# Optimization experiments

Measured on AMD Instinct MI355X. Metric: run time of the kernel, lower is better.

Reference implementation:

```python
import jax, jax.numpy as jnp
import numpy as np

N_NODES = 100000
N_EDGES = 600000
DIM = 128  # 2 * size_in


def gcn_layer(x, W, b, src, dst, n):
    # GCNConv (PyG, normalize=True, add_self_loops=True):
    # h = x @ W; norm = deg^-1/2[src] * deg^-1/2[dst] with self-loops; out = scatter_add + b
    h = x @ W
    loops = jnp.arange(n)
    s = jnp.concatenate([src, loops])
    d = jnp.concatenate([dst, loops])
    deg = jax.ops.segment_sum(jnp.ones_like(s, dtype=x.dtype), d, num_segments=n)
    dinv = jnp.where(deg > 0, deg ** -0.5, 0.0).astype(x.dtype)
    norm = dinv[s] * dinv[d]  # [E+N]
    msg = h[s] * norm[:, None]  # [E+N, DIM] -- dominant gather traffic
    out = jax.ops.segment_sum(msg, d, num_segments=n)
    return out + b


def setup_inputs() -> dict:
    key = jax.random.key(0)
    k = jax.random.split(key, 6)
    x = jax.random.normal(k[0], (N_NODES, DIM), dtype=jnp.float32)
    W1 = jax.random.normal(k[1], (DIM, DIM), dtype=jnp.float32) * (DIM ** -0.5)
    b1 = jax.random.normal(k[2], (DIM,), dtype=jnp.float32) * 0.02
    W2 = jax.random.normal(k[3], (DIM, DIM), dtype=jnp.float32) * (DIM ** -0.5)
    b2 = jax.random.normal(k[4], (DIM,), dtype=jnp.float32) * 0.02
    edge_index = jax.random.randint(k[5], (2, N_EDGES), 0, N_NODES, dtype=jnp.int64 if jax.config.jax_enable_x64 else jnp.int32)
    return {"x": x, "W1": W1, "b1": b1, "W2": W2, "b2": b2, "edge_index": edge_index}


def reference(x, W1, b1, W2, b2, edge_index):
    src, dst = edge_index[0], edge_index[1]
    out = gcn_layer(x, W1, b1, src, dst, N_NODES)
    out = jnp.tanh(out)
    out = gcn_layer(out, W2, b2, src, dst, N_NODES)
    return out
```

## Files before the change

### kernel.cpp

```cpp
#include <hip/hip_runtime.h>
#include <math.h>

#define NBLK 256

typedef __attribute__((ext_vector_type(8))) short short8v;
typedef __attribute__((ext_vector_type(4))) float f32x4;

__device__ __forceinline__ unsigned cvt_pk_bf16(float lo, float hi) {
    unsigned r;
    asm("v_cvt_pk_bf16_f32 %0, %1, %2" : "=v"(r) : "v"(lo), "v"(hi));
    return r;
}
__device__ __forceinline__ float bf_lo(unsigned u) { return __uint_as_float(u << 16); }
__device__ __forceinline__ float bf_hi(unsigned u) { return __uint_as_float(u & 0xffff0000u); }

__device__ __forceinline__ float fast_tanh(float x) {
    float cx = fminf(fmaxf(x, -15.f), 15.f);
    float e = __expf(2.f * cx);
    return (e - 1.f) / (e + 1.f);
}


__global__ __launch_bounds__(NBLK) void scan1_k(const int* __restrict__ cnt, int n,
                                                int* __restrict__ off, int* __restrict__ bsum) {
    __shared__ int ls[NBLK];
    int base = blockIdx.x * 1024 + threadIdx.x * 4;
    int v[4]; int s = 0;
#pragma unroll
    for (int i = 0; i < 4; ++i) {
        int idx = base + i;
        v[i] = (idx < n) ? cnt[idx] : 0;
        s += v[i];
    }
    ls[threadIdx.x] = s;
    __syncthreads();
    for (int o = 1; o < NBLK; o <<= 1) {
        int t = (threadIdx.x >= (unsigned)o) ? ls[threadIdx.x - o] : 0;
        __syncthreads();
        ls[threadIdx.x] += t;
        __syncthreads();
    }
    int run = ls[threadIdx.x] - s;
#pragma unroll
    for (int i = 0; i < 4; ++i) {
        int idx = base + i;
        if (idx < n) off[idx] = run;
        run += v[i];
    }
    if (threadIdx.x == NBLK - 1) bsum[blockIdx.x] = ls[NBLK - 1];
}

__global__ void scan2_k(int* bsum, int nb) {
    __shared__ int ls[128];
    int t = threadIdx.x;
    int v = (t < nb) ? bsum[t] : 0;
    ls[t] = v;
    __syncthreads();
    for (int o = 1; o < 128; o <<= 1) {
        int tv = (t >= o) ? ls[t - o] : 0;
        __syncthreads();
        ls[t] += tv;
        __syncthreads();
    }
    if (t < nb) bsum[t] = ls[t] - v;
}

__global__ __launch_bounds__(NBLK) void scan3_k(int* __restrict__ off, const int* __restrict__ bsum,
                                                const int* __restrict__ cnt,
                                                float* __restrict__ dinv, int n) {
    int i = blockIdx.x * blockDim.x + threadIdx.x;
    if (i < n) {
        off[i] += bsum[i >> 10];
        dinv[i] = rsqrtf((float)(cnt[i] + 1));
    }
}

__global__ __launch_bounds__(NBLK) void fill2_k(const int* __restrict__ src, const int* __restrict__ dst, int E,
                                                const int* __restrict__ off, const int* __restrict__ pos,
                                                int* __restrict__ srcs) {
    int e = blockIdx.x * blockDim.x + threadIdx.x;
    if (e >= E) return;
    srcs[off[dst[e]] + pos[e]] = src[e];
}

__global__ __launch_bounds__(NBLK) void wcast_k(const float* __restrict__ W1, const float* __restrict__ W2,
                                                ushort* __restrict__ Wt1, ushort* __restrict__ Wt2) {
    int i = blockIdx.x * blockDim.x + threadIdx.x;
    int which = i >> 14;
    int idx = i & 16383;
    const float* W = which ? W2 : W1;
    ushort* Wt = which ? Wt2 : Wt1;
    int k = idx >> 7, c = idx & 127;
    float v = W[idx];
    Wt[c * 128 + k] = (ushort)(cvt_pk_bf16(v, v) & 0xffffu);
}


template<int CVT, int DINV, int DO_COUNT>
__global__ __launch_bounds__(NBLK, 4) void gemm_mfma_k(const void* __restrict__ Xin,
                                                       const ushort* __restrict__ Wt,
                                                       const float* __restrict__ dinv,
                                                       ushort* __restrict__ Gb, int nrows,
                                                       const int* __restrict__ dste,
                                                       int* __restrict__ cntp,
                                                       int* __restrict__ posp, int E) {
    __shared__ unsigned Xls[64 * 64];
    __shared__ unsigned Wls[128 * 64];
    const int t = threadIdx.x;
    const int lane = t & 63;
    const int wv = t >> 6;
    const int l15 = lane & 15;
    const int g = lane >> 4;
    const int row0 = blockIdx.x * 64;

    {
        const uint4* Wv = (const uint4*)Wt;
        for (int i = t; i < 2048; i += NBLK) {
            int col = i >> 4, ku = i & 15;
            *(uint4*)&Wls[(col * 16 + (ku ^ (col & 15))) * 4] = Wv[i];
        }
    }
    {
        int r = t >> 2;
        int rg = row0 + r;
#pragma unroll
        for (int j = 0; j < 4; ++j) {
            int u = (t & 3) + 4 * j;
            uint4 val;
            if (CVT) {
                float4 f0 = make_float4(0.f,0.f,0.f,0.f), f1 = f0;
                if (rg < nrows) {
                    const float4* Xv = (const float4*)Xin;
                    f0 = Xv[(size_t)rg * 32 + u * 2];
                    f1 = Xv[(size_t)rg * 32 + u * 2 + 1];
                }
                val.x = cvt_pk_bf16(f0.x, f0.y); val.y = cvt_pk_bf16(f0.z, f0.w);
                val.z = cvt_pk_bf16(f1.x, f1.y); val.w = cvt_pk_bf16(f1.z, f1.w);
            } else {
                val = make_uint4(0u,0u,0u,0u);
                if (rg < nrows) val = ((const uint4*)Xin)[(size_t)rg * 16 + u];
            }
            *(uint4*)&Xls[(r * 16 + (u ^ (r & 15))) * 4] = val;
        }
    }
    __syncthreads();

    short8v A[4];
#pragma unroll
    for (int ks = 0; ks < 4; ++ks) {
        int r = wv * 16 + l15;
        int u = ks * 4 + g;
        A[ks] = *(short8v*)&Xls[(r * 16 + (u ^ (r & 15))) * 4];
    }

    f32x4 acc[8];
#pragma unroll
    for (int nt = 0; nt < 8; ++nt) acc[nt] = (f32x4){0.f, 0.f, 0.f, 0.f};
#pragma unroll
    for (int nt = 0; nt < 8; ++nt) {
        int col = nt * 16 + l15;
#pragma unroll
        for (int ks = 0; ks < 4; ++ks) {
            int ku = ks * 4 + g;
            short8v b = *(short8v*)&Wls[(col * 16 + (ku ^ (col & 15))) * 4];
            acc[nt] = __builtin_amdgcn_mfma_f32_16x16x32_bf16(A[ks], b, acc[nt], 0, 0, 0);
        }
    }

    int trow0 = row0 + wv * 16;
    float dv[4];
#pragma unroll
    for (int q = 0; q < 4; ++q) {
        int row = trow0 + g * 4 + q;
        dv[q] = DINV ? ((row < nrows) ? dinv[row] : 0.f) : 1.f;
    }
#pragma unroll
    for (int nt = 0; nt < 8; ++nt)
#pragma unroll
        for (int q = 0; q < 4; ++q) {
            int row = trow0 + g * 4 + q;
            if (row < nrows) {
                float val = DINV ? acc[nt][q] * dv[q] : acc[nt][q];
                Gb[(size_t)row * 128 + nt * 16 + l15] =
                    (ushort)(cvt_pk_bf16(val, val) & 0xffffu);
            }
        }

    if (DO_COUNT) {
        int stride = gridDim.x * NBLK;
        for (int e = blockIdx.x * NBLK + t; e < E; e += stride)
            posp[e] = atomicAdd(&cntp[dste[e]], 1);
    }
}


#define UPK_FMA(u4, nm, A) { \
    A[0] = fmaf(bf_lo((u4).x), (nm), A[0]); A[1] = fmaf(bf_hi((u4).x), (nm), A[1]); \
    A[2] = fmaf(bf_lo((u4).y), (nm), A[2]); A[3] = fmaf(bf_hi((u4).y), (nm), A[3]); \
    A[4] = fmaf(bf_lo((u4).z), (nm), A[4]); A[5] = fmaf(bf_hi((u4).z), (nm), A[5]); \
    A[6] = fmaf(bf_lo((u4).w), (nm), A[6]); A[7] = fmaf(bf_hi((u4).w), (nm), A[7]); }

template<int SRC_DINV, int TANH_, int OUT_BF16>
__global__ __launch_bounds__(NBLK, 4) void aggregate_k(const ushort* __restrict__ Gb,
                                                       const int* __restrict__ off, const int* __restrict__ cnt,
                                                       const int* __restrict__ srcs,
                                                       const float* __restrict__ dinv,
                                                       const float* __restrict__ bias,
                                                       void* __restrict__ outp, int n) {
    int node = (blockIdx.x * blockDim.x + threadIdx.x) >> 4;
    if (node >= n) return;
    int il = threadIdx.x & 15;

    const uint4* Gv = (const uint4*)Gb;
    float dvn = dinv[node];
    float sw = SRC_DINV ? dvn : 1.f;
    uint4 s0 = Gv[(size_t)node * 16 + il];
    float acc[8] = {
        bf_lo(s0.x) * sw, bf_hi(s0.x) * sw, bf_lo(s0.y) * sw, bf_hi(s0.y) * sw,
        bf_lo(s0.z) * sw, bf_hi(s0.z) * sw, bf_lo(s0.w) * sw, bf_hi(s0.w) * sw
    };

    int e0 = off[node];
    int deg = cnt[node];
    for (int b = 0; b < deg; b += 8) {
        int sidx[8]; float nm[8];
#pragma unroll
        for (int q = 0; q < 8; ++q) {
            bool v = (b + q) < deg;
            sidx[q] = v ? srcs[e0 + b + q] : node;
            nm[q] = v ? 1.f : 0.f;
        }
        if (SRC_DINV) {
#pragma unroll
            for (int q = 0; q < 8; ++q) nm[q] *= dinv[sidx[q]];
        }
        uint4 gr[8];
#pragma unroll
        for (int q = 0; q < 8; ++q) gr[q] = Gv[(size_t)sidx[q] * 16 + il];
#pragma unroll
        for (int q = 0; q < 8; ++q) UPK_FMA(gr[q], nm[q], acc);
    }

    float4 b0 = *(const float4*)&bias[il * 8];
    float4 b1 = *(const float4*)&bias[il * 8 + 4];
    float r[8];
    r[0] = fmaf(acc[0], dvn, b0.x); r[1] = fmaf(acc[1], dvn, b0.y);
    r[2] = fmaf(acc[2], dvn, b0.z); r[3] = fmaf(acc[3], dvn, b0.w);
    r[4] = fmaf(acc[4], dvn, b1.x); r[5] = fmaf(acc[5], dvn, b1.y);
    r[6] = fmaf(acc[6], dvn, b1.z); r[7] = fmaf(acc[7], dvn, b1.w);

    if (TANH_) {
#pragma unroll
        for (int i = 0; i < 8; ++i) r[i] = fast_tanh(r[i]);
    }

    if (OUT_BF16) {
        uint4 o;
        o.x = cvt_pk_bf16(r[0], r[1]); o.y = cvt_pk_bf16(r[2], r[3]);
        o.z = cvt_pk_bf16(r[4], r[5]); o.w = cvt_pk_bf16(r[6], r[7]);
        ((uint4*)outp)[(size_t)node * 16 + il] = o;
    } else {
        float* O = (float*)outp;
        *(float4*)&O[(size_t)node * 128 + il * 8]     = make_float4(r[0], r[1], r[2], r[3]);
        *(float4*)&O[(size_t)node * 128 + il * 8 + 4] = make_float4(r[4], r[5], r[6], r[7]);
    }
}


extern "C" void kernel_launch(void* const* d_in, const int* in_sizes, int n_in,
                              void* d_out, int out_size, void* d_ws, size_t ws_size,
                              hipStream_t stream) {
    const float* x  = (const float*)d_in[0];
    const float* W1 = (const float*)d_in[1];
    const float* b1 = (const float*)d_in[2];
    const float* W2 = (const float*)d_in[3];
    const float* b2 = (const float*)d_in[4];
    const int*   ei = (const int*)d_in[5];

    const int N = in_sizes[0] / 128;
    const int E = in_sizes[5] / 2;
    const int* src = ei;
    const int* dst = ei + E;

    char* p = (char*)d_ws;
    ushort* gb    = (ushort*)p; p += (size_t)N * 128 * sizeof(ushort);
    ushort* tb    = (ushort*)p; p += (size_t)N * 128 * sizeof(ushort);
    int*    cnt   = (int*)p;    p += (size_t)N * sizeof(int);
    int*    off   = (int*)p;    p += (size_t)N * sizeof(int);
    float*  dinv  = (float*)p;  p += (size_t)N * sizeof(float);
    int*    srcs  = (int*)p;    p += (size_t)E * sizeof(int);
    int*    pos   = (int*)p;    p += (size_t)E * sizeof(int);
    ushort* Wt1   = (ushort*)p; p += 16384 * sizeof(ushort);
    ushort* Wt2   = (ushort*)p; p += 16384 * sizeof(ushort);
    int*    bsum  = (int*)p;    p += 1024;

    const int nb  = (N + 1023) / 1024;
    const int nbt = (N + 63) / 64;
    const int agg_blocks = ((size_t)N * 16 + NBLK - 1) / NBLK;

    hipMemsetAsync(cnt, 0, (size_t)N * sizeof(int), stream);
    wcast_k<<<128, NBLK, 0, stream>>>(W1, W2, Wt1, Wt2);

    gemm_mfma_k<1, 0, 1><<<nbt, NBLK, 0, stream>>>(x, Wt1, nullptr, gb, N, dst, cnt, pos, E);

    scan1_k<<<nb, NBLK, 0, stream>>>(cnt, N, off, bsum);
    scan2_k<<<1, 128, 0, stream>>>(bsum, nb);
    scan3_k<<<(N + NBLK - 1) / NBLK, NBLK, 0, stream>>>(off, bsum, cnt, dinv, N);
    fill2_k<<<(E + NBLK - 1) / NBLK, NBLK, 0, stream>>>(src, dst, E, off, pos, srcs);

    aggregate_k<1, 1, 1><<<agg_blocks, NBLK, 0, stream>>>(gb, off, cnt, srcs, dinv, b1, tb, N);
    gemm_mfma_k<0, 1, 0><<<nbt, NBLK, 0, stream>>>(tb, Wt2, dinv, gb, N, nullptr, nullptr, nullptr, 0);
    aggregate_k<0, 0, 0><<<agg_blocks, NBLK, 0, stream>>>(gb, off, cnt, srcs, dinv, b2, d_out, N);
}
```

Before: 168.4 us.

## Split degree-count atomics across eight per-block-group counter slices

The edge-degree counting atomics in the first GEMM now go to one of eight counter arrays chosen by block index, with the slice id packed into the per-edge position. The scan sums the eight slices, and a new pass turns each slice into a base offset and writes a separate degree array, which the fill and aggregate kernels use. The aim is to cut atomic contention on the same counter addresses. In exchange it adds an 8x larger memset and extra strided reads and writes in the scan kernels.

```diff
diff --git a/kernel.cpp b/kernel.cpp
--- a/kernel.cpp
+++ b/kernel.cpp
@@ -21,7 +21,7 @@
 }
 
 
-__global__ __launch_bounds__(NBLK) void scan1_k(const int* __restrict__ cnt, int n,
+__global__ __launch_bounds__(NBLK) void scan1_k(const int* __restrict__ cnt8, int n,
                                                 int* __restrict__ off, int* __restrict__ bsum) {
     __shared__ int ls[NBLK];
     int base = blockIdx.x * 1024 + threadIdx.x * 4;
@@ -29,8 +29,13 @@
 #pragma unroll
     for (int i = 0; i < 4; ++i) {
         int idx = base + i;
-        v[i] = (idx < n) ? cnt[idx] : 0;
-        s += v[i];
+        int d = 0;
+        if (idx < n) {
+#pragma unroll
+            for (int x = 0; x < 8; ++x) d += cnt8[(size_t)x * n + idx];
+        }
+        v[i] = d;
+        s += d;
     }
     ls[threadIdx.x] = s;
     __syncthreads();
@@ -66,21 +71,33 @@
 }
 
 __global__ __launch_bounds__(NBLK) void scan3_k(int* __restrict__ off, const int* __restrict__ bsum,
-                                                const int* __restrict__ cnt,
+                                                int* __restrict__ cnt8, int* __restrict__ deg,
                                                 float* __restrict__ dinv, int n) {
     int i = blockIdx.x * blockDim.x + threadIdx.x;
     if (i < n) {
-        off[i] += bsum[i >> 10];
-        dinv[i] = rsqrtf((float)(cnt[i] + 1));
+        int o = off[i] + bsum[i >> 10];
+        off[i] = o;
+        int run = o;
+#pragma unroll
+        for (int x = 0; x < 8; ++x) {
+            size_t idx = (size_t)x * n + i;
+            int c = cnt8[idx];
+            cnt8[idx] = run;
+            run += c;
+        }
+        int d = run - o;
+        deg[i] = d;
+        dinv[i] = rsqrtf((float)(d + 1));
     }
 }
 
 __global__ __launch_bounds__(NBLK) void fill2_k(const int* __restrict__ src, const int* __restrict__ dst, int E,
-                                                const int* __restrict__ off, const int* __restrict__ pos,
-                                                int* __restrict__ srcs) {
+                                                const int* __restrict__ base8, const int* __restrict__ pos,
+                                                int* __restrict__ srcs, int n) {
     int e = blockIdx.x * blockDim.x + threadIdx.x;
     if (e >= E) return;
-    srcs[off[dst[e]] + pos[e]] = src[e];
+    int pe = pos[e];
+    srcs[base8[(size_t)(pe & 7) * n + dst[e]] + (pe >> 3)] = src[e];
 }
 
 __global__ __launch_bounds__(NBLK) void wcast_k(const float* __restrict__ W1, const float* __restrict__ W2,
@@ -102,7 +119,7 @@
                                                        const float* __restrict__ dinv,
                                                        ushort* __restrict__ Gb, int nrows,
                                                        const int* __restrict__ dste,
-                                                       int* __restrict__ cntp,
+                                                       int* __restrict__ cnt8,
                                                        int* __restrict__ posp, int E) {
     __shared__ unsigned Xls[64 * 64];
     __shared__ unsigned Wls[128 * 64];
@@ -187,9 +204,11 @@
         }
 
     if (DO_COUNT) {
+        const int part = blockIdx.x & 7;
+        int* cslice = cnt8 + (size_t)part * nrows;
         int stride = gridDim.x * NBLK;
         for (int e = blockIdx.x * NBLK + t; e < E; e += stride)
-            posp[e] = atomicAdd(&cntp[dste[e]], 1);
+            posp[e] = (atomicAdd(&cslice[dste[e]], 1) << 3) | part;
     }
 }
 
@@ -202,7 +221,7 @@
 
 template<int SRC_DINV, int TANH_, int OUT_BF16>
 __global__ __launch_bounds__(NBLK, 4) void aggregate_k(const ushort* __restrict__ Gb,
-                                                       const int* __restrict__ off, const int* __restrict__ cnt,
+                                                       const int* __restrict__ off, const int* __restrict__ deg_,
                                                        const int* __restrict__ srcs,
                                                        const float* __restrict__ dinv,
                                                        const float* __restrict__ bias,
@@ -221,7 +240,7 @@
     };
 
     int e0 = off[node];
-    int deg = cnt[node];
+    int deg = deg_[node];
     for (int b = 0; b < deg; b += 8) {
         int sidx[8]; float nm[8];
 #pragma unroll
@@ -285,8 +304,9 @@
     char* p = (char*)d_ws;
     ushort* gb    = (ushort*)p; p += (size_t)N * 128 * sizeof(ushort);
     ushort* tb    = (ushort*)p; p += (size_t)N * 128 * sizeof(ushort);
-    int*    cnt   = (int*)p;    p += (size_t)N * sizeof(int);
+    int*    cnt8  = (int*)p;    p += (size_t)8 * N * sizeof(int);
     int*    off   = (int*)p;    p += (size_t)N * sizeof(int);
+    int*    deg   = (int*)p;    p += (size_t)N * sizeof(int);
     float*  dinv  = (float*)p;  p += (size_t)N * sizeof(float);
     int*    srcs  = (int*)p;    p += (size_t)E * sizeof(int);
     int*    pos   = (int*)p;    p += (size_t)E * sizeof(int);
@@ -298,17 +318,17 @@
     const int nbt = (N + 63) / 64;
     const int agg_blocks = ((size_t)N * 16 + NBLK - 1) / NBLK;
 
-    hipMemsetAsync(cnt, 0, (size_t)N * sizeof(int), stream);
+    hipMemsetAsync(cnt8, 0, (size_t)8 * N * sizeof(int), stream);
     wcast_k<<<128, NBLK, 0, stream>>>(W1, W2, Wt1, Wt2);
 
-    gemm_mfma_k<1, 0, 1><<<nbt, NBLK, 0, stream>>>(x, Wt1, nullptr, gb, N, dst, cnt, pos, E);
-
-    scan1_k<<<nb, NBLK, 0, stream>>>(cnt, N, off, bsum);
+    gemm_mfma_k<1, 0, 1><<<nbt, NBLK, 0, stream>>>(x, Wt1, nullptr, gb, N, dst, cnt8, pos, E);
+
+    scan1_k<<<nb, NBLK, 0, stream>>>(cnt8, N, off, bsum);
     scan2_k<<<1, 128, 0, stream>>>(bsum, nb);
-    scan3_k<<<(N + NBLK - 1) / NBLK, NBLK, 0, stream>>>(off, bsum, cnt, dinv, N);
-    fill2_k<<<(E + NBLK - 1) / NBLK, NBLK, 0, stream>>>(src, dst, E, off, pos, srcs);
-
-    aggregate_k<1, 1, 1><<<agg_blocks, NBLK, 0, stream>>>(gb, off, cnt, srcs, dinv, b1, tb, N);
+    scan3_k<<<(N + NBLK - 1) / NBLK, NBLK, 0, stream>>>(off, bsum, cnt8, deg, dinv, N);
+    fill2_k<<<(E + NBLK - 1) / NBLK, NBLK, 0, stream>>>(src, dst, E, cnt8, pos, srcs, N);
+
+    aggregate_k<1, 1, 1><<<agg_blocks, NBLK, 0, stream>>>(gb, off, deg, srcs, dinv, b1, tb, N);
     gemm_mfma_k<0, 1, 0><<<nbt, NBLK, 0, stream>>>(tb, Wt2, dinv, gb, N, nullptr, nullptr, nullptr, 0);
-    aggregate_k<0, 0, 0><<<agg_blocks, NBLK, 0, stream>>>(gb, off, cnt, srcs, dinv, b2, d_out, N);
-}
+    aggregate_k<0, 0, 0><<<agg_blocks, NBLK, 0, stream>>>(gb, off, deg, srcs, dinv, b2, d_out, N);
+}
```

Measured after the change: 166.0 us. Within noise of the previous version (-1.5%).

## Build CSR via range-partitioned LDS histograms and load GEMM A operand directly

Applied to the files above, without the earlier changes.

Replaces global-atomic degree counting (fused into the first GEMM) and the pos/fill pass with two kernels. In each, a block owns a contiguous range of destination nodes and scans all edges, using shared-memory atomics for counting and for placing sources. This removes the memset and the per-edge pos array, at the cost of every block rereading the full edge list with only 32 blocks active. The GEMM also loads its A fragments straight from global memory instead of staging X through LDS.

```diff
diff --git a/kernel.cpp b/kernel.cpp
--- a/kernel.cpp
+++ b/kernel.cpp
@@ -2,6 +2,9 @@
 #include <math.h>
 
 #define NBLK 256
+#define HB   32
+#define HT   1024
+#define RMAX 3200
 
 typedef __attribute__((ext_vector_type(8))) short short8v;
 typedef __attribute__((ext_vector_type(4))) float f32x4;
@@ -18,6 +21,61 @@
     float cx = fminf(fmaxf(x, -15.f), 15.f);
     float e = __expf(2.f * cx);
     return (e - 1.f) / (e + 1.f);
+}
+
+
+__global__ __launch_bounds__(HT) void count_hist_k(const int* __restrict__ dst, int E,
+                                                   int* __restrict__ cnt, int n, int R) {
+    __shared__ int hist[RMAX];
+    const int base = blockIdx.x * R;
+    for (int j = threadIdx.x; j < R; j += HT) hist[j] = 0;
+    __syncthreads();
+    const int e4 = E >> 2;
+    const int4* d4 = (const int4*)dst;
+    for (int i = threadIdx.x; i < e4; i += HT) {
+        int4 d = d4[i];
+        int v;
+        v = d.x - base; if ((unsigned)v < (unsigned)R) atomicAdd(&hist[v], 1);
+        v = d.y - base; if ((unsigned)v < (unsigned)R) atomicAdd(&hist[v], 1);
+        v = d.z - base; if ((unsigned)v < (unsigned)R) atomicAdd(&hist[v], 1);
+        v = d.w - base; if ((unsigned)v < (unsigned)R) atomicAdd(&hist[v], 1);
+    }
+    for (int e = (e4 << 2) + threadIdx.x; e < E; e += HT) {
+        int v = dst[e] - base; if ((unsigned)v < (unsigned)R) atomicAdd(&hist[v], 1);
+    }
+    __syncthreads();
+    for (int j = threadIdx.x; j < R; j += HT) {
+        int b = base + j;
+        if (b < n) cnt[b] = hist[j];
+    }
+}
+
+__global__ __launch_bounds__(HT) void fill_hist_k(const int* __restrict__ src, const int* __restrict__ dst,
+                                                  int E, const int* __restrict__ off,
+                                                  int* __restrict__ srcs, int n, int R) {
+    __shared__ int cur[RMAX];
+    const int base = blockIdx.x * R;
+    for (int j = threadIdx.x; j < R; j += HT) {
+        int b = base + j;
+        cur[j] = (b < n) ? off[b] : 0;
+    }
+    __syncthreads();
+    const int e4 = E >> 2;
+    const int4* d4 = (const int4*)dst;
+    const int4* s4 = (const int4*)src;
+    for (int i = threadIdx.x; i < e4; i += HT) {
+        int4 d = d4[i];
+        int4 s = s4[i];
+        int v;
+        v = d.x - base; if ((unsigned)v < (unsigned)R) srcs[atomicAdd(&cur[v], 1)] = s.x;
+        v = d.y - base; if ((unsigned)v < (unsigned)R) srcs[atomicAdd(&cur[v], 1)] = s.y;
+        v = d.z - base; if ((unsigned)v < (unsigned)R) srcs[atomicAdd(&cur[v], 1)] = s.z;
+        v = d.w - base; if ((unsigned)v < (unsigned)R) srcs[atomicAdd(&cur[v], 1)] = s.w;
+    }
+    for (int e = (e4 << 2) + threadIdx.x; e < E; e += HT) {
+        int v = dst[e] - base;
+        if ((unsigned)v < (unsigned)R) srcs[atomicAdd(&cur[v], 1)] = src[e];
+    }
 }
 
 
@@ -73,14 +131,6 @@
         off[i] += bsum[i >> 10];
         dinv[i] = rsqrtf((float)(cnt[i] + 1));
     }
-}
-
-__global__ __launch_bounds__(NBLK) void fill2_k(const int* __restrict__ src, const int* __restrict__ dst, int E,
-                                                const int* __restrict__ off, const int* __restrict__ pos,
-                                                int* __restrict__ srcs) {
-    int e = blockIdx.x * blockDim.x + threadIdx.x;
-    if (e >= E) return;
-    srcs[off[dst[e]] + pos[e]] = src[e];
 }
 
 __global__ __launch_bounds__(NBLK) void wcast_k(const float* __restrict__ W1, const float* __restrict__ W2,
@@ -96,15 +146,11 @@
 }
 
 
-template<int CVT, int DINV, int DO_COUNT>
+template<int CVT, int DINV>
 __global__ __launch_bounds__(NBLK, 4) void gemm_mfma_k(const void* __restrict__ Xin,
                                                        const ushort* __restrict__ Wt,
                                                        const float* __restrict__ dinv,
-                                                       ushort* __restrict__ Gb, int nrows,
-                                                       const int* __restrict__ dste,
-                                                       int* __restrict__ cntp,
-                                                       int* __restrict__ posp, int E) {
-    __shared__ unsigned Xls[64 * 64];
+                                                       ushort* __restrict__ Gb, int nrows) {
     __shared__ unsigned Wls[128 * 64];
     const int t = threadIdx.x;
     const int lane = t & 63;
@@ -120,38 +166,32 @@
             *(uint4*)&Wls[(col * 16 + (ku ^ (col & 15))) * 4] = Wv[i];
         }
     }
-    {
-        int r = t >> 2;
-        int rg = row0 + r;
-#pragma unroll
-        for (int j = 0; j < 4; ++j) {
-            int u = (t & 3) + 4 * j;
-            uint4 val;
-            if (CVT) {
-                float4 f0 = make_float4(0.f,0.f,0.f,0.f), f1 = f0;
-                if (rg < nrows) {
-                    const float4* Xv = (const float4*)Xin;
-                    f0 = Xv[(size_t)rg * 32 + u * 2];
-                    f1 = Xv[(size_t)rg * 32 + u * 2 + 1];
-                }
-                val.x = cvt_pk_bf16(f0.x, f0.y); val.y = cvt_pk_bf16(f0.z, f0.w);
-                val.z = cvt_pk_bf16(f1.x, f1.y); val.w = cvt_pk_bf16(f1.z, f1.w);
-            } else {
-                val = make_uint4(0u,0u,0u,0u);
-                if (rg < nrows) val = ((const uint4*)Xin)[(size_t)rg * 16 + u];
-            }
-            *(uint4*)&Xls[(r * 16 + (u ^ (r & 15))) * 4] = val;
-        }
-    }
-    __syncthreads();
-
+
+    int arow = row0 + wv * 16 + l15;
+    int ar = (arow < nrows) ? arow : 0;
     short8v A[4];
-#pragma unroll
-    for (int ks = 0; ks < 4; ++ks) {
-        int r = wv * 16 + l15;
-        int u = ks * 4 + g;
-        A[ks] = *(short8v*)&Xls[(r * 16 + (u ^ (r & 15))) * 4];
-    }
+    if (CVT) {
+        const float4* Xv = (const float4*)Xin;
+#pragma unroll
+        for (int ks = 0; ks < 4; ++ks) {
+            float4 f0 = Xv[(size_t)ar * 32 + ks * 8 + g * 2];
+            float4 f1 = Xv[(size_t)ar * 32 + ks * 8 + g * 2 + 1];
+            union { uint4 u; short8v s; } c;
+            c.u.x = cvt_pk_bf16(f0.x, f0.y); c.u.y = cvt_pk_bf16(f0.z, f0.w);
+            c.u.z = cvt_pk_bf16(f1.x, f1.y); c.u.w = cvt_pk_bf16(f1.z, f1.w);
+            A[ks] = c.s;
+        }
+    } else {
+        const uint4* Xu = (const uint4*)Xin;
+#pragma unroll
+        for (int ks = 0; ks < 4; ++ks) {
+            union { uint4 u; short8v s; } c;
+            c.u = Xu[(size_t)ar * 16 + ks * 4 + g];
+            A[ks] = c.s;
+        }
+    }
+
+    __syncthreads();
 
     f32x4 acc[8];
 #pragma unroll
@@ -185,12 +225,6 @@
                     (ushort)(cvt_pk_bf16(val, val) & 0xffffu);
             }
         }
-
-    if (DO_COUNT) {
-        int stride = gridDim.x * NBLK;
-        for (int e = blockIdx.x * NBLK + t; e < E; e += stride)
-            posp[e] = atomicAdd(&cntp[dste[e]], 1);
-    }
 }
 
 
@@ -202,7 +236,7 @@
 
 template<int SRC_DINV, int TANH_, int OUT_BF16>
 __global__ __launch_bounds__(NBLK, 4) void aggregate_k(const ushort* __restrict__ Gb,
-                                                       const int* __restrict__ off, const int* __restrict__ cnt,
+                                                       const int* __restrict__ off, const int* __restrict__ deg_,
                                                        const int* __restrict__ srcs,
                                                        const float* __restrict__ dinv,
                                                        const float* __restrict__ bias,
@@ -221,7 +255,7 @@
     };
 
     int e0 = off[node];
-    int deg = cnt[node];
+    int deg = deg_[node];
     for (int b = 0; b < deg; b += 8) {
         int sidx[8]; float nm[8];
 #pragma unroll
@@ -289,26 +323,26 @@
     int*    off   = (int*)p;    p += (size_t)N * sizeof(int);
     float*  dinv  = (float*)p;  p += (size_t)N * sizeof(float);
     int*    srcs  = (int*)p;    p += (size_t)E * sizeof(int);
-    int*    pos   = (int*)p;    p += (size_t)E * sizeof(int);
     ushort* Wt1   = (ushort*)p; p += 16384 * sizeof(ushort);
     ushort* Wt2   = (ushort*)p; p += 16384 * sizeof(ushort);
     int*    bsum  = (int*)p;    p += 1024;
 
     const int nb  = (N + 1023) / 1024;
     const int nbt = (N + 63) / 64;
+    const int R   = (N + HB - 1) / HB;
     const int agg_blocks = ((size_t)N * 16 + NBLK - 1) / NBLK;
 
-    hipMemsetAsync(cnt, 0, (size_t)N * sizeof(int), stream);
     wcast_k<<<128, NBLK, 0, stream>>>(W1, W2, Wt1, Wt2);
 
-    gemm_mfma_k<1, 0, 1><<<nbt, NBLK, 0, stream>>>(x, Wt1, nullptr, gb, N, dst, cnt, pos, E);
-
+    gemm_mfma_k<1, 0><<<nbt, NBLK, 0, stream>>>(x, Wt1, nullptr, gb, N);
+
+    count_hist_k<<<HB, HT, 0, stream>>>(dst, E, cnt, N, R);
     scan1_k<<<nb, NBLK, 0, stream>>>(cnt, N, off, bsum);
     scan2_k<<<1, 128, 0, stream>>>(bsum, nb);
     scan3_k<<<(N + NBLK - 1) / NBLK, NBLK, 0, stream>>>(off, bsum, cnt, dinv, N);
-    fill2_k<<<(E + NBLK - 1) / NBLK, NBLK, 0, stream>>>(src, dst, E, off, pos, srcs);
+    fill_hist_k<<<HB, HT, 0, stream>>>(src, dst, E, off, srcs, N, R);
 
     aggregate_k<1, 1, 1><<<agg_blocks, NBLK, 0, stream>>>(gb, off, cnt, srcs, dinv, b1, tb, N);
-    gemm_mfma_k<0, 1, 0><<<nbt, NBLK, 0, stream>>>(tb, Wt2, dinv, gb, N, nullptr, nullptr, nullptr, 0);
+    gemm_mfma_k<0, 1><<<nbt, NBLK, 0, stream>>>(tb, Wt2, dinv, gb, N);
     aggregate_k<0, 0, 0><<<agg_blocks, NBLK, 0, stream>>>(gb, off, cnt, srcs, dinv, b2, d_out, N);
 }
```

After: 306.1 us. +81.8%, slower.

## Split degree counting into its own kernel and load GEMM A-operands directly to registers

Applied to the files above, without the earlier changes.

Moves the per-edge atomic degree counting out of the first GEMM kernel into a separate count_k launch. The GEMM now loads its X rows straight from global memory into MFMA A-fragment registers instead of staging them through a swizzled shared-memory tile, which drops the X LDS buffer and its extra reads. This cuts shared-memory use and may raise occupancy. The cost is an extra kernel launch, the loss of overlap between counting and the GEMM, and less coalesced global loads for the A-fragments.

```diff
diff --git a/kernel.cpp b/kernel.cpp
--- a/kernel.cpp
+++ b/kernel.cpp
@@ -18,6 +18,21 @@
     float cx = fminf(fmaxf(x, -15.f), 15.f);
     float e = __expf(2.f * cx);
     return (e - 1.f) / (e + 1.f);
+}
+
+
+__global__ __launch_bounds__(NBLK) void count_k(const int* __restrict__ dst, int E,
+                                                int* __restrict__ cnt, int* __restrict__ pos) {
+    int e = blockIdx.x * blockDim.x + threadIdx.x;
+    if (e < E) pos[e] = atomicAdd(&cnt[dst[e]], 1);
+}
+
+__global__ __launch_bounds__(NBLK) void fill2_k(const int* __restrict__ src, const int* __restrict__ dst, int E,
+                                                const int* __restrict__ off, const int* __restrict__ pos,
+                                                int* __restrict__ srcs) {
+    int e = blockIdx.x * blockDim.x + threadIdx.x;
+    if (e >= E) return;
+    srcs[off[dst[e]] + pos[e]] = src[e];
 }
 
 
@@ -75,14 +90,6 @@
     }
 }
 
-__global__ __launch_bounds__(NBLK) void fill2_k(const int* __restrict__ src, const int* __restrict__ dst, int E,
-                                                const int* __restrict__ off, const int* __restrict__ pos,
-                                                int* __restrict__ srcs) {
-    int e = blockIdx.x * blockDim.x + threadIdx.x;
-    if (e >= E) return;
-    srcs[off[dst[e]] + pos[e]] = src[e];
-}
-
 __global__ __launch_bounds__(NBLK) void wcast_k(const float* __restrict__ W1, const float* __restrict__ W2,
                                                 ushort* __restrict__ Wt1, ushort* __restrict__ Wt2) {
     int i = blockIdx.x * blockDim.x + threadIdx.x;
@@ -96,15 +103,11 @@
 }
 
 
-template<int CVT, int DINV, int DO_COUNT>
+template<int CVT, int DINV>
 __global__ __launch_bounds__(NBLK, 4) void gemm_mfma_k(const void* __restrict__ Xin,
                                                        const ushort* __restrict__ Wt,
                                                        const float* __restrict__ dinv,
-                                                       ushort* __restrict__ Gb, int nrows,
-                                                       const int* __restrict__ dste,
-                                                       int* __restrict__ cntp,
-                                                       int* __restrict__ posp, int E) {
-    __shared__ unsigned Xls[64 * 64];
+                                                       ushort* __restrict__ Gb, int nrows) {
     __shared__ unsigned Wls[128 * 64];
     const int t = threadIdx.x;
     const int lane = t & 63;
@@ -120,38 +123,32 @@
             *(uint4*)&Wls[(col * 16 + (ku ^ (col & 15))) * 4] = Wv[i];
         }
     }
-    {
-        int r = t >> 2;
-        int rg = row0 + r;
-#pragma unroll
-        for (int j = 0; j < 4; ++j) {
-            int u = (t & 3) + 4 * j;
-            uint4 val;
-            if (CVT) {
-                float4 f0 = make_float4(0.f,0.f,0.f,0.f), f1 = f0;
-                if (rg < nrows) {
-                    const float4* Xv = (const float4*)Xin;
-                    f0 = Xv[(size_t)rg * 32 + u * 2];
-                    f1 = Xv[(size_t)rg * 32 + u * 2 + 1];
-                }
-                val.x = cvt_pk_bf16(f0.x, f0.y); val.y = cvt_pk_bf16(f0.z, f0.w);
-                val.z = cvt_pk_bf16(f1.x, f1.y); val.w = cvt_pk_bf16(f1.z, f1.w);
-            } else {
-                val = make_uint4(0u,0u,0u,0u);
-                if (rg < nrows) val = ((const uint4*)Xin)[(size_t)rg * 16 + u];
-            }
-            *(uint4*)&Xls[(r * 16 + (u ^ (r & 15))) * 4] = val;
-        }
-    }
+
+    int arow = row0 + wv * 16 + l15;
+    int ar = (arow < nrows) ? arow : 0;
+    short8v A[4];
+    if (CVT) {
+        const float4* Xv = (const float4*)Xin;
+#pragma unroll
+        for (int ks = 0; ks < 4; ++ks) {
+            float4 f0 = Xv[(size_t)ar * 32 + ks * 8 + g * 2];
+            float4 f1 = Xv[(size_t)ar * 32 + ks * 8 + g * 2 + 1];
+            union { uint4 u; short8v s; } c;
+            c.u.x = cvt_pk_bf16(f0.x, f0.y); c.u.y = cvt_pk_bf16(f0.z, f0.w);
+            c.u.z = cvt_pk_bf16(f1.x, f1.y); c.u.w = cvt_pk_bf16(f1.z, f1.w);
+            A[ks] = c.s;
+        }
+    } else {
+        const uint4* Xu = (const uint4*)Xin;
+#pragma unroll
+        for (int ks = 0; ks < 4; ++ks) {
+            union { uint4 u; short8v s; } c;
+            c.u = Xu[(size_t)ar * 16 + ks * 4 + g];
+            A[ks] = c.s;
+        }
+    }
+
     __syncthreads();
-
-    short8v A[4];
-#pragma unroll
-    for (int ks = 0; ks < 4; ++ks) {
-        int r = wv * 16 + l15;
-        int u = ks * 4 + g;
-        A[ks] = *(short8v*)&Xls[(r * 16 + (u ^ (r & 15))) * 4];
-    }
 
     f32x4 acc[8];
 #pragma unroll
@@ -185,12 +182,6 @@
                     (ushort)(cvt_pk_bf16(val, val) & 0xffffu);
             }
         }
-
-    if (DO_COUNT) {
-        int stride = gridDim.x * NBLK;
-        for (int e = blockIdx.x * NBLK + t; e < E; e += stride)
-            posp[e] = atomicAdd(&cntp[dste[e]], 1);
-    }
 }
 
 
@@ -202,7 +193,7 @@
 
 template<int SRC_DINV, int TANH_, int OUT_BF16>
 __global__ __launch_bounds__(NBLK, 4) void aggregate_k(const ushort* __restrict__ Gb,
-                                                       const int* __restrict__ off, const int* __restrict__ cnt,
+                                                       const int* __restrict__ off, const int* __restrict__ deg_,
                                                        const int* __restrict__ srcs,
                                                        const float* __restrict__ dinv,
                                                        const float* __restrict__ bias,
@@ -221,7 +212,7 @@
     };
 
     int e0 = off[node];
-    int deg = cnt[node];
+    int deg = deg_[node];
     for (int b = 0; b < deg; b += 8) {
         int sidx[8]; float nm[8];
 #pragma unroll
@@ -301,7 +292,9 @@
     hipMemsetAsync(cnt, 0, (size_t)N * sizeof(int), stream);
     wcast_k<<<128, NBLK, 0, stream>>>(W1, W2, Wt1, Wt2);
 
-    gemm_mfma_k<1, 0, 1><<<nbt, NBLK, 0, stream>>>(x, Wt1, nullptr, gb, N, dst, cnt, pos, E);
+    count_k<<<(E + NBLK - 1) / NBLK, NBLK, 0, stream>>>(dst, E, cnt, pos);
+
+    gemm_mfma_k<1, 0><<<nbt, NBLK, 0, stream>>>(x, Wt1, nullptr, gb, N);
 
     scan1_k<<<nb, NBLK, 0, stream>>>(cnt, N, off, bsum);
     scan2_k<<<1, 128, 0, stream>>>(bsum, nb);
@@ -309,6 +302,6 @@
     fill2_k<<<(E + NBLK - 1) / NBLK, NBLK, 0, stream>>>(src, dst, E, off, pos, srcs);
 
     aggregate_k<1, 1, 1><<<agg_blocks, NBLK, 0, stream>>>(gb, off, cnt, srcs, dinv, b1, tb, N);
-    gemm_mfma_k<0, 1, 0><<<nbt, NBLK, 0, stream>>>(tb, Wt2, dinv, gb, N, nullptr, nullptr, nullptr, 0);
+    gemm_mfma_k<0, 1><<<nbt, NBLK, 0, stream>>>(tb, Wt2, dinv, gb, N);
     aggregate_k<0, 0, 0><<<agg_blocks, NBLK, 0, stream>>>(gb, off, cnt, srcs, dinv, b2, d_out, N);
 }
```

After: 157.8 us. 1.07x faster.
